# Optimization experiments

Hardware: AMD Instinct MI355X
Metric: run time of the kernel (lower is better)

## Reference

```python
import jax, jax.numpy as jnp
import numpy as np

N = 100000   # nodes
E = 1600000  # edges
IN_CH = 128
EDGE_DIM = 16
HEADS = 4
OUT_CH = 16
NEG_SLOPE = 0.2


def setup_inputs() -> dict:
    key = jax.random.key(0)
    ks = jax.random.split(key, 12)
    HC = HEADS * OUT_CH
    inp = {
        "x": jax.random.normal(ks[0], (N, IN_CH), dtype=jnp.float32),
        "edge_index": jax.random.randint(ks[1], (2, E), 0, N, dtype=jnp.int32),
        "edge_attr": jax.random.normal(ks[2], (E, EDGE_DIM), dtype=jnp.float32),
        # linear layer params (W stored as [in, out] so y = x @ W + b)
        "W_src": jax.random.normal(ks[3], (IN_CH, HC), dtype=jnp.float32) / np.sqrt(IN_CH),
        "b_src": jnp.zeros((HC,), dtype=jnp.float32),
        "W_dst": jax.random.normal(ks[4], (IN_CH, HC), dtype=jnp.float32) / np.sqrt(IN_CH),
        "b_dst": jnp.zeros((HC,), dtype=jnp.float32),
        "W_edge": jax.random.normal(ks[5], (EDGE_DIM, HC), dtype=jnp.float32) / np.sqrt(EDGE_DIM),
        "b_edge": jnp.zeros((HC,), dtype=jnp.float32),
        # attention vectors [1, heads, out_channels]
        "att_src": jax.random.normal(ks[6], (1, HEADS, OUT_CH), dtype=jnp.float32) * 0.1,
        "att_dst": jax.random.normal(ks[7], (1, HEADS, OUT_CH), dtype=jnp.float32) * 0.1,
        "att_edge": jax.random.normal(ks[8], (1, HEADS, OUT_CH), dtype=jnp.float32) * 0.1,
    }
    return inp


def _segment_softmax(alpha, seg, num_segments):
    # alpha: [E, H]; softmax over edges sharing the same dst node (seg).
    m = jax.ops.segment_max(alpha, seg, num_segments=num_segments)
    m = jnp.where(jnp.isfinite(m), m, 0.0)  # empty segments -> -inf; neutralize
    a = jnp.exp(alpha - m[seg])
    s = jax.ops.segment_sum(a, seg, num_segments=num_segments)
    return a / (s[seg] + 1e-16)


def reference(x, edge_index, edge_attr, W_src, b_src, W_dst, b_dst,
              W_edge, b_edge, att_src, att_dst, att_edge):
    n = x.shape[0]
    src_idx, dst_idx = edge_index[0], edge_index[1]

    src = (x @ W_src + b_src).reshape(n, HEADS, OUT_CH)        # [N,H,C]
    dst = (x @ W_dst + b_dst).reshape(n, HEADS, OUT_CH)        # [N,H,C]
    edge_feat = (edge_attr @ W_edge + b_edge).reshape(-1, HEADS, OUT_CH)  # [E,H,C]

    alpha_src = jnp.sum(src * att_src, axis=-1)[src_idx]       # [E,H]
    alpha_dst = jnp.sum(dst * att_dst, axis=-1)[dst_idx]       # [E,H]
    alpha_edge = jnp.sum(edge_feat * att_edge, axis=-1)        # [E,H]

    alpha = alpha_src + alpha_dst + alpha_edge
    alpha = jnp.where(alpha >= 0, alpha, NEG_SLOPE * alpha)    # leaky_relu(0.2)
    alpha = _segment_softmax(alpha, dst_idx, n)                # [E,H]
    # dropout is identity in eval mode

    msg = src[src_idx] * alpha[..., None]                      # [E,H,C]
    out = jax.ops.segment_sum(msg, dst_idx, num_segments=n)    # [N,H,C]
    return out.reshape(n, HEADS * OUT_CH)
```

## Files before the change

### kernel.cpp

```cpp
#include <hip/hip_runtime.h>


#define N_NODES 100000
#define N_EDGES 1600000
#define SCAN_B 1024
#define SCAN_NBLK ((N_NODES + SCAN_B - 1) / SCAN_B)

__global__ __launch_bounds__(256) void k_node_proj(
    const float* __restrict__ x, const float* __restrict__ Wsrc,
    const float* __restrict__ bsrc, const float* __restrict__ Wdst,
    const float* __restrict__ bdst, const float* __restrict__ att_src,
    const float* __restrict__ att_dst, float* __restrict__ src_proj,
    float* __restrict__ alpha_sn, float* __restrict__ alpha_dn)
{
    __shared__ float xs[32 * 128];
    const int tid = threadIdx.x;
    const int nbase = blockIdx.x * 32;

    const float4* xsrc = (const float4*)(x + (size_t)nbase * 128);
    float4* xd = (float4*)xs;
#pragma unroll
    for (int i = 0; i < 4; ++i)
        xd[tid + i * 256] = xsrc[tid + i * 256];
    __syncthreads();

    const int col = tid & 63;
    const int g = tid >> 6;

    float accS[8], accD[8];
#pragma unroll
    for (int i = 0; i < 8; ++i) { accS[i] = 0.f; accD[i] = 0.f; }

    for (int k4 = 0; k4 < 128; k4 += 4) {
        float4 xv[8];
#pragma unroll
        for (int i = 0; i < 8; ++i)
            xv[i] = *(const float4*)&xs[(g * 8 + i) * 128 + k4];
#pragma unroll
        for (int kk = 0; kk < 4; ++kk) {
            float wsv = Wsrc[(k4 + kk) * 64 + col];
            float wdv = Wdst[(k4 + kk) * 64 + col];
#pragma unroll
            for (int i = 0; i < 8; ++i) {
                float xvk = ((const float*)&xv[i])[kk];
                accS[i] = fmaf(xvk, wsv, accS[i]);
                accD[i] = fmaf(xvk, wdv, accD[i]);
            }
        }
    }

    const float bs = bsrc[col], bd = bdst[col];
    const float as_ = att_src[col], ad_ = att_dst[col];
    const int h = col >> 4;
#pragma unroll
    for (int i = 0; i < 8; ++i) {
        const int n = nbase + g * 8 + i;
        float vS = accS[i] + bs;
        float vD = accD[i] + bd;
        src_proj[(size_t)n * 64 + col] = vS;
        float t1 = vS * as_;
        float t2 = vD * ad_;
#pragma unroll
        for (int off = 8; off >= 1; off >>= 1) {
            t1 += __shfl_xor(t1, off, 16);
            t2 += __shfl_xor(t2, off, 16);
        }
        if ((col & 15) == 0) {
            alpha_sn[n * 4 + h] = t1;
            alpha_dn[n * 4 + h] = t2;
        }
    }
}

__global__ void k_prep(const float* __restrict__ We, const float* __restrict__ be,
                       const float* __restrict__ att_e, float* __restrict__ V)
{
    const int t = threadIdx.x;
    const int k = t >> 2, h = t & 3;
    float acc = 0.f;
    for (int c = 0; c < 16; ++c)
        acc += We[k * 64 + h * 16 + c] * att_e[h * 16 + c];
    V[k * 4 + h] = acc;
    if (t < 4) {
        float b = 0.f;
        for (int c = 0; c < 16; ++c)
            b += be[t * 16 + c] * att_e[t * 16 + c];
        V[64 + t] = b;
    }
}

__global__ __launch_bounds__(256) void k_hist(const int* __restrict__ ei,
                                               int* __restrict__ cnt)
{
    const int e = blockIdx.x * 256 + threadIdx.x;
    if (e >= N_EDGES) return;
    atomicAdd(&cnt[ei[N_EDGES + e]], 1);
}

__global__ __launch_bounds__(256) void k_scan_part(const int* __restrict__ cnt,
                                                    int* __restrict__ partial)
{
    __shared__ int red[4];
    const int t = threadIdx.x;
    const int base = blockIdx.x * SCAN_B + t * 4;
    int s = 0;
#pragma unroll
    for (int i = 0; i < 4; ++i) {
        const int idx = base + i;
        if (idx < N_NODES) s += cnt[idx];
    }
#pragma unroll
    for (int off = 32; off >= 1; off >>= 1)
        s += __shfl_xor(s, off, 64);
    if ((t & 63) == 0) red[t >> 6] = s;
    __syncthreads();
    if (t == 0)
        partial[blockIdx.x] = red[0] + red[1] + red[2] + red[3];
}

__global__ __launch_bounds__(128) void k_scan_top(int* __restrict__ partial)
{
    __shared__ int sums[128];
    const int t = threadIdx.x;
    sums[t] = (t < SCAN_NBLK) ? partial[t] : 0;
    __syncthreads();
#pragma unroll
    for (int off = 1; off < 128; off <<= 1) {
        int v = (t >= off) ? sums[t - off] : 0;
        __syncthreads();
        sums[t] += v;
        __syncthreads();
    }
    if (t < SCAN_NBLK) partial[t] = (t == 0) ? 0 : sums[t - 1];
}

__global__ __launch_bounds__(256) void k_scan_down(
    const int* __restrict__ cnt, const int* __restrict__ partial,
    int* __restrict__ row_start, int* __restrict__ cursor)
{
    __shared__ int tsum[256];
    const int t = threadIdx.x;
    const int base = blockIdx.x * SCAN_B + t * 4;
    int c[4];
#pragma unroll
    for (int i = 0; i < 4; ++i) {
        const int idx = base + i;
        c[i] = (idx < N_NODES) ? cnt[idx] : 0;
    }
    const int tot = c[0] + c[1] + c[2] + c[3];
    tsum[t] = tot;
    __syncthreads();
#pragma unroll
    for (int off = 1; off < 256; off <<= 1) {
        int v = (t >= off) ? tsum[t - off] : 0;
        __syncthreads();
        tsum[t] += v;
        __syncthreads();
    }
    int run = partial[blockIdx.x] + ((t == 0) ? 0 : tsum[t - 1]);
#pragma unroll
    for (int i = 0; i < 4; ++i) {
        const int idx = base + i;
        if (idx < N_NODES) {
            row_start[idx] = run;
            cursor[idx] = run;
        }
        run += c[i];
    }
    if (blockIdx.x == 0 && t == 0)
        row_start[N_NODES] = N_EDGES;
}

__global__ __launch_bounds__(256) void k_fill(
    const int* __restrict__ ei, const float* __restrict__ ea,
    const float* __restrict__ V, const float* __restrict__ alpha_sn,
    const float* __restrict__ alpha_dn, int* __restrict__ cursor,
    int* __restrict__ rec_src, float4* __restrict__ rec_w)
{
    __shared__ float Vs[68];
    if (threadIdx.x < 68) Vs[threadIdx.x] = V[threadIdx.x];
    __syncthreads();

    const int e = blockIdx.x * 256 + threadIdx.x;
    if (e >= N_EDGES) return;
    const int src = ei[e];
    const int dst = ei[N_EDGES + e];

    const float4* ea4 = (const float4*)(ea + (size_t)e * 16);
    float ek[16];
    {
        float4 c0 = ea4[0], c1 = ea4[1], c2 = ea4[2], c3 = ea4[3];
        ek[0]=c0.x; ek[1]=c0.y; ek[2]=c0.z; ek[3]=c0.w;
        ek[4]=c1.x; ek[5]=c1.y; ek[6]=c1.z; ek[7]=c1.w;
        ek[8]=c2.x; ek[9]=c2.y; ek[10]=c2.z; ek[11]=c2.w;
        ek[12]=c3.x; ek[13]=c3.y; ek[14]=c3.z; ek[15]=c3.w;
    }
    float a[4] = {Vs[64], Vs[65], Vs[66], Vs[67]};
#pragma unroll
    for (int k = 0; k < 16; ++k) {
#pragma unroll
        for (int h = 0; h < 4; ++h)
            a[h] = fmaf(ek[k], Vs[k * 4 + h], a[h]);
    }

    const float4 asn = *(const float4*)(alpha_sn + (size_t)src * 4);
    const float4 adn = *(const float4*)(alpha_dn + (size_t)dst * 4);
    float a0 = a[0] + asn.x + adn.x;
    float a1 = a[1] + asn.y + adn.y;
    float a2 = a[2] + asn.z + adn.z;
    float a3 = a[3] + asn.w + adn.w;
    a0 = (a0 >= 0.f) ? a0 : 0.2f * a0;
    a1 = (a1 >= 0.f) ? a1 : 0.2f * a1;
    a2 = (a2 >= 0.f) ? a2 : 0.2f * a2;
    a3 = (a3 >= 0.f) ? a3 : 0.2f * a3;

    const int slot = atomicAdd(&cursor[dst], 1);
    rec_src[slot] = src;
    rec_w[slot] = make_float4(__expf(a0), __expf(a1), __expf(a2), __expf(a3));
}

__global__ __launch_bounds__(256) void k_gather(
    const int* __restrict__ row_start, const int* __restrict__ rec_src,
    const float* __restrict__ rec_w, const float* __restrict__ src_proj,
    float* __restrict__ out)
{
    const int lane = threadIdx.x & 63;
    const int node = (blockIdx.x * 256 + threadIdx.x) >> 6;
    const int h = lane >> 4;
    const int base = row_start[node];
    const int end = row_start[node + 1];

    float acc = 0.f, denom = 0.f;
    for (int j = base; j < end; ++j) {
        const int src = rec_src[j];
        const float wv = rec_w[(size_t)j * 4 + h];
        const float v = src_proj[(size_t)src * 64 + lane];
        denom += wv;
        acc = fmaf(wv, v, acc);
    }
    out[(size_t)node * 64 + lane] = acc / (denom + 1e-16f);
}

extern "C" void kernel_launch(void* const* d_in, const int* in_sizes, int n_in,
                              void* d_out, int out_size, void* d_ws, size_t ws_size,
                              hipStream_t stream) {
    const float* x     = (const float*)d_in[0];
    const int*   ei    = (const int*)d_in[1];
    const float* ea    = (const float*)d_in[2];
    const float* Wsrc  = (const float*)d_in[3];
    const float* bsrc  = (const float*)d_in[4];
    const float* Wdst  = (const float*)d_in[5];
    const float* bdst  = (const float*)d_in[6];
    const float* We    = (const float*)d_in[7];
    const float* be    = (const float*)d_in[8];
    const float* att_s = (const float*)d_in[9];
    const float* att_d = (const float*)d_in[10];
    const float* att_e = (const float*)d_in[11];
    float* out = (float*)d_out;

    float* wsf      = (float*)d_ws;
    float* src_proj = wsf;
    float* alpha_sn = src_proj + (size_t)N_NODES * 64;
    float* alpha_dn = alpha_sn + (size_t)N_NODES * 4;
    float* rec_w    = alpha_dn + (size_t)N_NODES * 4;
    int*   rec_src  = (int*)(rec_w + (size_t)N_EDGES * 4);
    int*   cnt      = rec_src + N_EDGES;
    int*   row_start= cnt + N_NODES;
    int*   cursor   = row_start + N_NODES + 4;
    int*   partial  = cursor + N_NODES;
    float* V        = (float*)(partial + 128);

    hipMemsetAsync(cnt, 0, (size_t)N_NODES * sizeof(int), stream);

    k_node_proj<<<N_NODES / 32, 256, 0, stream>>>(x, Wsrc, bsrc, Wdst, bdst,
                                                  att_s, att_d, src_proj,
                                                  alpha_sn, alpha_dn);
    k_prep<<<1, 64, 0, stream>>>(We, be, att_e, V);
    k_hist<<<N_EDGES / 256, 256, 0, stream>>>(ei, cnt);
    k_scan_part<<<SCAN_NBLK, 256, 0, stream>>>(cnt, partial);
    k_scan_top<<<1, 128, 0, stream>>>(partial);
    k_scan_down<<<SCAN_NBLK, 256, 0, stream>>>(cnt, partial, row_start, cursor);
    k_fill<<<N_EDGES / 256, 256, 0, stream>>>(ei, ea, V, alpha_sn, alpha_dn,
                                              cursor, rec_src, (float4*)rec_w);
    k_gather<<<(N_NODES * 64) / 256, 256, 0, stream>>>(row_start, rec_src,
                                                       rec_w, src_proj, out);
}
```

Measured before the change: 587.3 us.

## Store source projections and edge weights in bf16, pack edge records, unroll gather

Source node projections are stored as bf16 instead of fp32, which halves the bytes read in the random gather. Edge records now hold the source index and four bf16 exp-weights in a single int4 store/load, replacing two separate arrays. The gather loop is unrolled by four to issue several independent loads at once. This costs some accuracy from bf16 rounding of both the features and the unnormalized softmax weights.

```diff
diff --git a/kernel.cpp b/kernel.cpp
--- a/kernel.cpp
+++ b/kernel.cpp
@@ -6,11 +6,19 @@
 #define SCAN_B 1024
 #define SCAN_NBLK ((N_NODES + SCAN_B - 1) / SCAN_B)
 
+static __device__ __forceinline__ unsigned int f2bf(float f) {
+    unsigned int u = __float_as_uint(f);
+    return (u + 0x7fffu + ((u >> 16) & 1u)) >> 16;
+}
+static __device__ __forceinline__ float bf2f(unsigned int bits16) {
+    return __uint_as_float(bits16 << 16);
+}
+
 __global__ __launch_bounds__(256) void k_node_proj(
     const float* __restrict__ x, const float* __restrict__ Wsrc,
     const float* __restrict__ bsrc, const float* __restrict__ Wdst,
     const float* __restrict__ bdst, const float* __restrict__ att_src,
-    const float* __restrict__ att_dst, float* __restrict__ src_proj,
+    const float* __restrict__ att_dst, unsigned short* __restrict__ spbf,
     float* __restrict__ alpha_sn, float* __restrict__ alpha_dn)
 {
     __shared__ float xs[32 * 128];
@@ -57,7 +65,7 @@
         const int n = nbase + g * 8 + i;
         float vS = accS[i] + bs;
         float vD = accD[i] + bd;
-        src_proj[(size_t)n * 64 + col] = vS;
+        spbf[(size_t)n * 64 + col] = (unsigned short)f2bf(vS);
         float t1 = vS * as_;
         float t2 = vD * ad_;
 #pragma unroll
@@ -175,7 +183,7 @@
     const int* __restrict__ ei, const float* __restrict__ ea,
     const float* __restrict__ V, const float* __restrict__ alpha_sn,
     const float* __restrict__ alpha_dn, int* __restrict__ cursor,
-    int* __restrict__ rec_src, float4* __restrict__ rec_w)
+    int4* __restrict__ rec)
 {
     __shared__ float Vs[68];
     if (threadIdx.x < 68) Vs[threadIdx.x] = V[threadIdx.x];
@@ -214,15 +222,16 @@
     a2 = (a2 >= 0.f) ? a2 : 0.2f * a2;
     a3 = (a3 >= 0.f) ? a3 : 0.2f * a3;
 
+    const unsigned int w01 = f2bf(__expf(a0)) | (f2bf(__expf(a1)) << 16);
+    const unsigned int w23 = f2bf(__expf(a2)) | (f2bf(__expf(a3)) << 16);
+
     const int slot = atomicAdd(&cursor[dst], 1);
-    rec_src[slot] = src;
-    rec_w[slot] = make_float4(__expf(a0), __expf(a1), __expf(a2), __expf(a3));
+    rec[slot] = make_int4(src, (int)w01, (int)w23, 0);
 }
 
 __global__ __launch_bounds__(256) void k_gather(
-    const int* __restrict__ row_start, const int* __restrict__ rec_src,
-    const float* __restrict__ rec_w, const float* __restrict__ src_proj,
-    float* __restrict__ out)
+    const int* __restrict__ row_start, const int4* __restrict__ rec,
+    const unsigned short* __restrict__ spbf, float* __restrict__ out)
 {
     const int lane = threadIdx.x & 63;
     const int node = (blockIdx.x * 256 + threadIdx.x) >> 6;
@@ -231,13 +240,30 @@
     const int end = row_start[node + 1];
 
     float acc = 0.f, denom = 0.f;
-    for (int j = base; j < end; ++j) {
-        const int src = rec_src[j];
-        const float wv = rec_w[(size_t)j * 4 + h];
-        const float v = src_proj[(size_t)src * 64 + lane];
-        denom += wv;
-        acc = fmaf(wv, v, acc);
-    }
+    int j = base;
+    for (; j + 4 <= end; j += 4) {
+        const int4 r0 = rec[j], r1 = rec[j + 1], r2 = rec[j + 2], r3 = rec[j + 3];
+        const float v0 = bf2f(spbf[((size_t)r0.x << 6) + lane]);
+        const float v1 = bf2f(spbf[((size_t)r1.x << 6) + lane]);
+        const float v2 = bf2f(spbf[((size_t)r2.x << 6) + lane]);
+        const float v3 = bf2f(spbf[((size_t)r3.x << 6) + lane]);
+#define WEXT(r) bf2f(((h & 1) ? ((unsigned int)((h < 2) ? r.y : r.z) >> 16) \
+                              : ((unsigned int)((h < 2) ? r.y : r.z) & 0xffffu)))
+        const float w0 = WEXT(r0), w1 = WEXT(r1), w2 = WEXT(r2), w3 = WEXT(r3);
+        denom += (w0 + w1) + (w2 + w3);
+        acc = fmaf(w0, v0, acc);
+        acc = fmaf(w1, v1, acc);
+        acc = fmaf(w2, v2, acc);
+        acc = fmaf(w3, v3, acc);
+    }
+    for (; j < end; ++j) {
+        const int4 r0 = rec[j];
+        const float v0 = bf2f(spbf[((size_t)r0.x << 6) + lane]);
+        const float w0 = WEXT(r0);
+        denom += w0;
+        acc = fmaf(w0, v0, acc);
+    }
+#undef WEXT
     out[(size_t)node * 64 + lane] = acc / (denom + 1e-16f);
 }
 
@@ -258,22 +284,20 @@
     const float* att_e = (const float*)d_in[11];
     float* out = (float*)d_out;
 
-    float* wsf      = (float*)d_ws;
-    float* src_proj = wsf;
-    float* alpha_sn = src_proj + (size_t)N_NODES * 64;
-    float* alpha_dn = alpha_sn + (size_t)N_NODES * 4;
-    float* rec_w    = alpha_dn + (size_t)N_NODES * 4;
-    int*   rec_src  = (int*)(rec_w + (size_t)N_EDGES * 4);
-    int*   cnt      = rec_src + N_EDGES;
-    int*   row_start= cnt + N_NODES;
-    int*   cursor   = row_start + N_NODES + 4;
-    int*   partial  = cursor + N_NODES;
-    float* V        = (float*)(partial + 128);
+    int4*  rec       = (int4*)d_ws;
+    unsigned short* spbf = (unsigned short*)(rec + N_EDGES);
+    float* alpha_sn  = (float*)(spbf + (size_t)N_NODES * 64);
+    float* alpha_dn  = alpha_sn + (size_t)N_NODES * 4;
+    int*   cnt       = (int*)(alpha_dn + (size_t)N_NODES * 4);
+    int*   row_start = cnt + N_NODES;
+    int*   cursor    = row_start + N_NODES + 4;
+    int*   partial   = cursor + N_NODES;
+    float* V         = (float*)(partial + 128);
 
     hipMemsetAsync(cnt, 0, (size_t)N_NODES * sizeof(int), stream);
 
     k_node_proj<<<N_NODES / 32, 256, 0, stream>>>(x, Wsrc, bsrc, Wdst, bdst,
-                                                  att_s, att_d, src_proj,
+                                                  att_s, att_d, spbf,
                                                   alpha_sn, alpha_dn);
     k_prep<<<1, 64, 0, stream>>>(We, be, att_e, V);
     k_hist<<<N_EDGES / 256, 256, 0, stream>>>(ei, cnt);
@@ -281,7 +305,6 @@
     k_scan_top<<<1, 128, 0, stream>>>(partial);
     k_scan_down<<<SCAN_NBLK, 256, 0, stream>>>(cnt, partial, row_start, cursor);
     k_fill<<<N_EDGES / 256, 256, 0, stream>>>(ei, ea, V, alpha_sn, alpha_dn,
-                                              cursor, rec_src, (float4*)rec_w);
-    k_gather<<<(N_NODES * 64) / 256, 256, 0, stream>>>(row_start, rec_src,
-                                                       rec_w, src_proj, out);
-}
+                                              cursor, rec);
+    k_gather<<<(N_NODES + 3) / 4, 256, 0, stream>>>(row_start, rec, spbf, out);
+}
```

Result: faster. 484.9 us (-17.4%).
